# Performance work log

Measured on AMD Instinct MI355X. Metric: run time of the kernel, lower is better.

The kernel has to match this reference:

```python
import jax, jax.numpy as jnp
import numpy as np

B, T, D = 4, 2048, 1024
H = 16
HD = D // H  # 64


def setup_inputs() -> dict:
    key = jax.random.key(0)
    ks = jax.random.split(key, 6)
    s = 0.02
    x = jax.random.normal(ks[0], (B, T, D), dtype=jnp.float32)
    # per-head projection weights, stored stacked: [H, HD, D] (torch Linear weight layout)
    Wq = jax.random.normal(ks[1], (H, HD, D), dtype=jnp.float32) * s
    Wk = jax.random.normal(ks[2], (H, HD, D), dtype=jnp.float32) * s
    Wv = jax.random.normal(ks[3], (H, HD, D), dtype=jnp.float32) * s
    Wo = jax.random.normal(ks[4], (D, D), dtype=jnp.float32) * s  # proj weight [out, in]
    bo = jax.random.normal(ks[5], (D,), dtype=jnp.float32) * s
    return {"x": x, "Wq": Wq, "Wk": Wk, "Wv": Wv, "Wo": Wo, "bo": bo}


def reference(x, Wq, Wk, Wv, Wo, bo):
    Bx, Tx, _ = x.shape
    # project: [B,T,D] x [H,HD,D] -> [B,H,T,HD]
    q = jnp.einsum('btd,hed->bhte', x, Wq)
    k = jnp.einsum('btd,hed->bhte', x, Wk)
    v = jnp.einsum('btd,hed->bhte', x, Wv)
    scale = 1.0 / jnp.sqrt(jnp.array(q.shape[-1], dtype=x.dtype))
    scores = jnp.einsum('bhte,bhse->bhts', q, k) * scale  # [B,H,T,T]
    causal = jnp.tril(jnp.ones((Tx, Tx), dtype=bool))
    scores = jnp.where(causal, scores, jnp.array(-jnp.inf, dtype=scores.dtype))
    weights = jax.nn.softmax(scores, axis=-1)
    out = jnp.einsum('bhts,bhse->bhte', weights, v)  # [B,H,T,HD]
    # concat heads (head h occupies contiguous slice, matching torch.cat order)
    out = out.transpose(0, 2, 1, 3).reshape(Bx, Tx, -1)  # [B,T,D]
    out = out @ Wo.T + bo
    return out
```

## Files before the change

### kernel.cpp

```cpp
#include <hip/hip_runtime.h>
#include <cstdint>
#include <cstddef>

typedef unsigned short u16;
typedef float  f32x4  __attribute__((ext_vector_type(4)));
typedef __bf16 bf16x8 __attribute__((ext_vector_type(8)));
typedef unsigned short us8 __attribute__((ext_vector_type(8)));
typedef unsigned short us4 __attribute__((ext_vector_type(4)));
typedef float  f32x4v __attribute__((ext_vector_type(4)));
typedef unsigned int u32x2 __attribute__((ext_vector_type(2)));

#define AS1 __attribute__((address_space(1)))
#define AS3 __attribute__((address_space(3)))

__device__ __forceinline__ u16 f2b(float f) {
  unsigned u = __float_as_uint(f);
  u += 0x7FFFu + ((u >> 16) & 1u);
  return (u16)(u >> 16);
}

__device__ __forceinline__ unsigned pkbf(float a, float b) {
  unsigned ua = __float_as_uint(a) + 0x8000u;
  unsigned ub = __float_as_uint(b) + 0x8000u;
  return __builtin_amdgcn_perm(ub, ua, 0x07060302u);
}

__device__ __forceinline__ unsigned cvtpk(float a, float b) {
  unsigned short lo = __builtin_bit_cast(unsigned short, (__bf16)a);
  unsigned short hi = __builtin_bit_cast(unsigned short, (__bf16)b);
  return (unsigned)lo | ((unsigned)hi << 16);
}

__device__ __forceinline__ bf16x8 ldfrag(const u16* p) {
  us8 v = *(const us8*)p;
  return __builtin_bit_cast(bf16x8, v);
}

__device__ __forceinline__ f32x4 mfma16(bf16x8 a, bf16x8 b, f32x4 c) {
  return __builtin_amdgcn_mfma_f32_16x16x32_bf16(a, b, c, 0, 0, 0);
}

__device__ __forceinline__ void gl_lds16(const u16* g, AS3 u16* l) {
  __builtin_amdgcn_global_load_lds((AS1 void*)g, (AS3 void*)l, 16, 0, 0);
}


__global__ __launch_bounds__(256) void cvt_all(
    const float* __restrict__ x,
    const float* __restrict__ Wq, const float* __restrict__ Wk,
    const float* __restrict__ Wv, const float* __restrict__ Wo,
    u16* __restrict__ xb, u16* __restrict__ Wqkv, u16* __restrict__ Wob) {
  for (int blk = blockIdx.x; blk < 12288; blk += 3072) {
    const float* s;
    u16* d;
    int i;
    if (blk < 8192)       { s = x;  d = xb;             i = blk * 256 + threadIdx.x; }
    else if (blk < 9216)  { s = Wq; d = Wqkv;           i = (blk - 8192) * 256 + threadIdx.x; }
    else if (blk < 10240) { s = Wk; d = Wqkv + 1048576; i = (blk - 9216) * 256 + threadIdx.x; }
    else if (blk < 11264) { s = Wv; d = Wqkv + 2097152; i = (blk - 10240) * 256 + threadIdx.x; }
    else                  { s = Wo; d = Wob;            i = (blk - 11264) * 256 + threadIdx.x; }
    f32x4v f = ((const f32x4v*)s)[i];
    us4 o = { f2b(f[0]), f2b(f[1]), f2b(f[2]), f2b(f[3]) };
    ((us4*)d)[i] = o;
  }
}

__global__ __launch_bounds__(256) void gemm_qkv(
    const u16* __restrict__ A, const u16* __restrict__ W,
    u16* __restrict__ Qb, u16* __restrict__ Kb, u16* __restrict__ Vt) {
  __shared__ u16 lA[128 * 64];
  __shared__ u16 lB[128 * 64];
  const int tid = threadIdx.x;
  const int lane = tid & 63, wave = tid >> 6;
  const int quad = lane >> 4, l16 = lane & 15;
  const int wr = wave >> 1, wc = wave & 1;

  const int p = blockIdx.x;
  const int l = (p & 7) * 64 + (p >> 3);
  const int by = l >> 3;
  const int bx0 = l & 7;
  const int m0 = by * 128;

  AS3 u16* lA3 = (AS3 u16*)lA;
  AS3 u16* lB3 = (AS3 u16*)lB;
  const int g3 = (((lane & 7) ^ (lane >> 3)) * 8);
  const int srow = lane >> 3;
  const int pA = ((quad) ^ (l16 & 7)) * 8;
  const int pB = ((4 + quad) ^ (l16 & 7)) * 8;

  const u16* gA = A + (size_t)(m0 + wave * 8 + srow) * 1024 + g3;

#pragma unroll 1
  for (int sec = 0; sec < 3; sec++) {
    const int n0 = (bx0 + sec * 8) * 128;
    const u16* gB = W + (size_t)(n0 + wave * 8 + srow) * 1024 + g3;
    f32x4 acc[4][4] = {};

    for (int k0 = 0; k0 < 1024; k0 += 64) {
      __syncthreads();
#pragma unroll
      for (int i = 0; i < 4; i++) {
        gl_lds16(gA + (size_t)i * 32768 + k0, lA3 + (i * 4 + wave) * 512);
        gl_lds16(gB + (size_t)i * 32768 + k0, lB3 + (i * 4 + wave) * 512);
      }
      __syncthreads();
#pragma unroll
      for (int kk = 0; kk < 2; kk++) {
        const int pk = kk ? pB : pA;
        bf16x8 aF[4], bF[4];
#pragma unroll
        for (int mt = 0; mt < 4; mt++)
          aF[mt] = ldfrag(&lA[(wr * 64 + mt * 16 + l16) * 64 + pk]);
#pragma unroll
        for (int nt = 0; nt < 4; nt++)
          bF[nt] = ldfrag(&lB[(wc * 64 + nt * 16 + l16) * 64 + pk]);
        if (sec != 2) {
#pragma unroll
          for (int mt = 0; mt < 4; mt++)
#pragma unroll
            for (int nt = 0; nt < 4; nt++)
              acc[mt][nt] = mfma16(bF[nt], aF[mt], acc[mt][nt]);
        } else {
#pragma unroll
          for (int mt = 0; mt < 4; mt++)
#pragma unroll
            for (int nt = 0; nt < 4; nt++)
              acc[mt][nt] = mfma16(aF[mt], bF[nt], acc[mt][nt]);
        }
      }
    }

    if (sec != 2) {
      const float qsc = (sec == 0) ? 0.180336880111120426f : 1.0f;
      u16* __restrict__ D = (sec == 0) ? Qb : Kb;
      const int hb = ((n0 & 1023) >> 6) + wc;
#pragma unroll
      for (int mt = 0; mt < 4; mt++) {
        int t = m0 + wr * 64 + mt * 16 + l16;
        int b = t >> 11, tt = t & 2047;
        size_t rowb = (((size_t)b * 16 + hb) * 2048 + tt) * 64;
#pragma unroll
        for (int nt = 0; nt < 4; nt++) {
          int e = nt * 16 + quad * 4;
          u32x2 pk = { pkbf(acc[mt][nt][0] * qsc, acc[mt][nt][1] * qsc),
                       pkbf(acc[mt][nt][2] * qsc, acc[mt][nt][3] * qsc) };
          *(u32x2*)&D[rowb + e] = pk;
        }
      }
    } else {
#pragma unroll
      for (int mt = 0; mt < 4; mt++) {
        int t = m0 + wr * 64 + mt * 16 + quad * 4;
        int b = t >> 11, tt = t & 2047;
#pragma unroll
        for (int nt = 0; nt < 4; nt++) {
          int ns = (n0 & 1023) + wc * 64 + nt * 16 + l16;
          int h = ns >> 6, e = ns & 63;
          size_t addr = (((size_t)b * 16 + h) * 64 + e) * 2048 + tt;
          u32x2 pk = { pkbf(acc[mt][nt][0], acc[mt][nt][1]),
                       pkbf(acc[mt][nt][2], acc[mt][nt][3]) };
          *(u32x2*)&Vt[addr] = pk;
        }
      }
    }
  }
}

__global__ __launch_bounds__(512, 4) void attn(
    const u16* __restrict__ Q, const u16* __restrict__ K,
    const u16* __restrict__ Vt, u16* __restrict__ O) {
  __shared__ u16 lK[128 * 64];
  __shared__ u16 lV[64 * 128];
  __shared__ u16 lP[8 * 16 * 40];
  const int tid = threadIdx.x;
  const int lane = tid & 63, wave = tid >> 6;
  const int quad = lane >> 4, l16 = lane & 15;
  const int bh = blockIdx.x;
  const int pidx = blockIdx.y;
  const size_t base = (size_t)bh * (2048 * 64);
  u16* lPw = lP + wave * 640;
  const int b = bh >> 4, h = bh & 15;
  AS3 u16* lK3 = (AS3 u16*)lK;
  AS3 u16* lV3 = (AS3 u16*)lV;

  const int g3 = ((lane & 7) ^ (lane >> 3)) * 8;
  const u16* gK = K + base + (size_t)(wave * 16 + (lane >> 3)) * 64 + g3;
  const int er = lane >> 4, p16 = lane & 15;
  const int e0 = wave * 8 + er, e1 = wave * 8 + 4 + er;
  const u16* gV0 = Vt + base + (size_t)e0 * 2048 + ((p16 ^ (e0 & 7)) * 8);
  const u16* gV1 = Vt + base + (size_t)e1 * 2048 + ((p16 ^ (e1 & 7)) * 8);

  const int e7 = l16 & 7;
  const int pq0 = (quad ^ e7) * 8;
  const int pq1 = ((4 + quad) ^ e7) * 8;

  us8 ones_u = { 0x3F80, 0x3F80, 0x3F80, 0x3F80, 0x3F80, 0x3F80, 0x3F80, 0x3F80 };
  const bf16x8 onesA = __builtin_bit_cast(bf16x8, ones_u);

  for (int half = 0; half < 2; half++) {
    const int qb = half ? pidx : (15 - pidx);
    const int t0 = qb << 7;
    const int tq = t0 + wave * 16 + l16;
    const bf16x8 qF0 = ldfrag(Q + base + (size_t)tq * 64 + quad * 8);
    const bf16x8 qF1 = ldfrag(Q + base + (size_t)tq * 64 + 32 + quad * 8);
    float l_i = 0.f;
    f32x4 o[4] = {};

    for (int j = 0; j <= qb; j++) {
      const int s0 = j << 7;
      __syncthreads();
      gl_lds16(gK + (size_t)s0 * 64,       lK3 + wave * 1024);
      gl_lds16(gK + (size_t)s0 * 64 + 512, lK3 + wave * 1024 + 512);
      gl_lds16(gV0 + s0, lV3 + wave * 1024);
      gl_lds16(gV1 + s0, lV3 + wave * 1024 + 512);
      __syncthreads();

      f32x4 S[8];
      __builtin_amdgcn_s_setprio(1);
#pragma unroll
      for (int nt = 0; nt < 8; nt++) {
        int sr = nt * 16 + l16;
        f32x4 a = {};
        a = mfma16(ldfrag(&lK[sr * 64 + pq0]), qF0, a);
        a = mfma16(ldfrag(&lK[sr * 64 + pq1]), qF1, a);
        S[nt] = a;
      }
      __builtin_amdgcn_s_setprio(0);

      if (j == qb) {
#pragma unroll
        for (int nt = 0; nt < 8; nt++)
#pragma unroll
          for (int r = 0; r < 4; r++) {
            int s = s0 + nt * 16 + quad * 4 + r;
            if (s > tq) S[nt][r] = -INFINITY;
          }
      }

#pragma unroll
      for (int nt = 0; nt < 8; nt++)
#pragma unroll
        for (int r = 0; r < 4; r++)
          S[nt][r] = __builtin_amdgcn_exp2f(S[nt][r]);

      f32x4 ol = {};
#pragma unroll
      for (int c = 0; c < 4; c++) {
        u32x2 d0 = { cvtpk(S[2*c][0],   S[2*c][1]),   cvtpk(S[2*c][2],   S[2*c][3]) };
        u32x2 d1 = { cvtpk(S[2*c+1][0], S[2*c+1][1]), cvtpk(S[2*c+1][2], S[2*c+1][3]) };
        *(u32x2*)&lPw[l16 * 40 + quad * 4]      = d0;
        *(u32x2*)&lPw[l16 * 40 + 16 + quad * 4] = d1;
        __asm__ volatile("s_waitcnt lgkmcnt(0)" ::: "memory");
        bf16x8 bP = ldfrag(&lPw[l16 * 40 + quad * 8]);
        __builtin_amdgcn_s_setprio(1);
#pragma unroll
        for (int ot = 0; ot < 4; ot++) {
          int pos = ((c * 4 + quad) ^ e7) * 8;
          o[ot] = mfma16(ldfrag(&lV[(ot * 16 + l16) * 128 + pos]), bP, o[ot]);
        }
        ol = mfma16(onesA, bP, ol);
        __builtin_amdgcn_s_setprio(0);
      }
      l_i += ol[0];
    }

    const float inv = 1.f / l_i;
#pragma unroll
    for (int ot = 0; ot < 4; ot++) {
      u32x2 pk = { cvtpk(o[ot][0] * inv, o[ot][1] * inv),
                   cvtpk(o[ot][2] * inv, o[ot][3] * inv) };
      *(u32x2*)&O[((size_t)b * 2048 + tq) * 1024 + h * 64 + ot * 16 + quad * 4] = pk;
    }
  }
}

__global__ __launch_bounds__(256) void gemm_out(
    const u16* __restrict__ A, const u16* __restrict__ W,
    const float* __restrict__ bias, float* __restrict__ out) {
  __shared__ u16 lA[128 * 64];
  __shared__ u16 lB[128 * 64];
  const int tid = threadIdx.x;
  const int lane = tid & 63, wave = tid >> 6;
  const int quad = lane >> 4, l16 = lane & 15;
  const int wr = wave >> 1, wc = wave & 1;
  const int m0 = blockIdx.y * 128;
  const int n0 = blockIdx.x * 128;
  AS3 u16* lA3 = (AS3 u16*)lA;
  AS3 u16* lB3 = (AS3 u16*)lB;
  f32x4 acc[4][4] = {};
  const int g3 = (((lane & 7) ^ (lane >> 3)) * 8);
  const int srow = lane >> 3;
  const int pA = ((quad) ^ (l16 & 7)) * 8;
  const int pB = ((4 + quad) ^ (l16 & 7)) * 8;
  const u16* gA = A + (size_t)(m0 + wave * 8 + srow) * 1024 + g3;
  const u16* gB = W + (size_t)(n0 + wave * 8 + srow) * 1024 + g3;

  for (int k0 = 0; k0 < 1024; k0 += 64) {
    __syncthreads();
#pragma unroll
    for (int i = 0; i < 4; i++) {
      gl_lds16(gA + (size_t)i * 32768 + k0, lA3 + (i * 4 + wave) * 512);
      gl_lds16(gB + (size_t)i * 32768 + k0, lB3 + (i * 4 + wave) * 512);
    }
    __syncthreads();
#pragma unroll
    for (int kk = 0; kk < 2; kk++) {
      const int pk = kk ? pB : pA;
      bf16x8 aF[4], bF[4];
#pragma unroll
      for (int mt = 0; mt < 4; mt++)
        aF[mt] = ldfrag(&lA[(wr * 64 + mt * 16 + l16) * 64 + pk]);
#pragma unroll
      for (int nt = 0; nt < 4; nt++)
        bF[nt] = ldfrag(&lB[(wc * 64 + nt * 16 + l16) * 64 + pk]);
#pragma unroll
      for (int mt = 0; mt < 4; mt++)
#pragma unroll
        for (int nt = 0; nt < 4; nt++)
          acc[mt][nt] = mfma16(aF[mt], bF[nt], acc[mt][nt]);
    }
  }

#pragma unroll
  for (int mt = 0; mt < 4; mt++) {
#pragma unroll
    for (int nt = 0; nt < 4; nt++) {
#pragma unroll
      for (int r = 0; r < 4; r++) {
        int m = m0 + wr * 64 + mt * 16 + quad * 4 + r;
        int n = n0 + wc * 64 + nt * 16 + l16;
        out[(size_t)m * 1024 + n] = acc[mt][nt][r] + bias[n];
      }
    }
  }
}

extern "C" void kernel_launch(void* const* d_in, const int* in_sizes, int n_in,
                              void* d_out, int out_size, void* d_ws, size_t ws_size,
                              hipStream_t stream) {
  const float* x  = (const float*)d_in[0];
  const float* Wq = (const float*)d_in[1];
  const float* Wk = (const float*)d_in[2];
  const float* Wv = (const float*)d_in[3];
  const float* Wo = (const float*)d_in[4];
  const float* bo = (const float*)d_in[5];
  float* out = (float*)d_out;

  u16* ws   = (u16*)d_ws;
  u16* xb   = ws;
  u16* Wqkv = ws + 8388608;
  u16* Wob  = ws + 11534336;
  u16* Qb   = ws + 12582912;
  u16* Ao   = xb;
  u16* Kb   = (u16*)d_out;
  u16* Vt   = Kb + 8388608;

  cvt_all<<<3072, 256, 0, stream>>>(x, Wq, Wk, Wv, Wo, xb, Wqkv, Wob);
  gemm_qkv<<<512, 256, 0, stream>>>(xb, Wqkv, Qb, Kb, Vt);
  attn<<<dim3(64, 8), 512, 0, stream>>>(Qb, Kb, Vt, Ao);
  gemm_out<<<dim3(8, 64), 256, 0, stream>>>(Ao, Wob, bo, out);
}
```

Measured before the change: 236.4 us.

## Double-buffer LDS in QKV and output GEMMs to overlap loads with MFMA

Both projection GEMMs now use two LDS buffers: the global-to-LDS load for the next K-tile is issued before computing on the current one, with one vmcnt wait and barrier per step instead of two syncthreads. The QKV GEMM flattens its three sections and sixteen K-steps into a single 48-step pipelined loop, so loads also run ahead across the section epilogue boundaries. This is meant to hide global load latency behind MFMA work. In exchange LDS per block doubles to 64KB, which may lower occupancy, and the waits rely on hand-placed sched barriers.

```diff
diff --git a/kernel.cpp b/kernel.cpp
--- a/kernel.cpp
+++ b/kernel.cpp
@@ -43,6 +43,9 @@
 __device__ __forceinline__ void gl_lds16(const u16* g, AS3 u16* l) {
   __builtin_amdgcn_global_load_lds((AS1 void*)g, (AS3 void*)l, 16, 0, 0);
 }
+
+#define SBAR0() __builtin_amdgcn_sched_barrier(0)
+#define WVM0()  do { __asm__ volatile("s_waitcnt vmcnt(0)" ::: "memory"); SBAR0(); } while (0)
 
 
 __global__ __launch_bounds__(256) void cvt_all(
@@ -68,8 +71,8 @@
 __global__ __launch_bounds__(256) void gemm_qkv(
     const u16* __restrict__ A, const u16* __restrict__ W,
     u16* __restrict__ Qb, u16* __restrict__ Kb, u16* __restrict__ Vt) {
-  __shared__ u16 lA[128 * 64];
-  __shared__ u16 lB[128 * 64];
+  __shared__ u16 lA[2 * 128 * 64];
+  __shared__ u16 lB[2 * 128 * 64];
   const int tid = threadIdx.x;
   const int lane = tid & 63, wave = tid >> 6;
   const int quad = lane >> 4, l16 = lane & 15;
@@ -89,81 +92,105 @@
   const int pB = ((4 + quad) ^ (l16 & 7)) * 8;
 
   const u16* gA = A + (size_t)(m0 + wave * 8 + srow) * 1024 + g3;
+  const u16* gW = W + (size_t)(wave * 8 + srow) * 1024 + g3;
+
+#define STAGE_T(T) do {                                                     \
+    int sec_ = (T) >> 4;                                                    \
+    int k0_ = ((T) & 15) * 64;                                              \
+    int bo_ = ((T) & 1) * 8192;                                             \
+    const u16* gBp_ = gW + (size_t)((bx0 + sec_ * 8) * 128) * 1024 + k0_;   \
+    const u16* gAp_ = gA + k0_;                                             \
+    _Pragma("unroll") for (int i_ = 0; i_ < 4; i_++) {                      \
+      gl_lds16(gAp_ + (size_t)i_ * 32768, lA3 + bo_ + (i_ * 4 + wave) * 512); \
+      gl_lds16(gBp_ + (size_t)i_ * 32768, lB3 + bo_ + (i_ * 4 + wave) * 512); \
+    }                                                                       \
+    SBAR0();                                                                \
+  } while (0)
+
+  f32x4 acc[4][4] = {};
+
+  STAGE_T(0);
+  WVM0();
+  __builtin_amdgcn_s_barrier();
+  SBAR0();
 
 #pragma unroll 1
-  for (int sec = 0; sec < 3; sec++) {
-    const int n0 = (bx0 + sec * 8) * 128;
-    const u16* gB = W + (size_t)(n0 + wave * 8 + srow) * 1024 + g3;
-    f32x4 acc[4][4] = {};
-
-    for (int k0 = 0; k0 < 1024; k0 += 64) {
-      __syncthreads();
-#pragma unroll
-      for (int i = 0; i < 4; i++) {
-        gl_lds16(gA + (size_t)i * 32768 + k0, lA3 + (i * 4 + wave) * 512);
-        gl_lds16(gB + (size_t)i * 32768 + k0, lB3 + (i * 4 + wave) * 512);
-      }
-      __syncthreads();
-#pragma unroll
-      for (int kk = 0; kk < 2; kk++) {
-        const int pk = kk ? pB : pA;
-        bf16x8 aF[4], bF[4];
+  for (int T = 0; T < 48; T++) {
+    if (T < 47) STAGE_T(T + 1);
+    const int sec = T >> 4;
+    const u16* bA = lA + (T & 1) * 8192;
+    const u16* bB = lB + (T & 1) * 8192;
+#pragma unroll
+    for (int kk = 0; kk < 2; kk++) {
+      const int pk = kk ? pB : pA;
+      bf16x8 aF[4], bF[4];
+#pragma unroll
+      for (int mt = 0; mt < 4; mt++)
+        aF[mt] = ldfrag(&bA[(wr * 64 + mt * 16 + l16) * 64 + pk]);
+#pragma unroll
+      for (int nt = 0; nt < 4; nt++)
+        bF[nt] = ldfrag(&bB[(wc * 64 + nt * 16 + l16) * 64 + pk]);
+      if (sec != 2) {
 #pragma unroll
         for (int mt = 0; mt < 4; mt++)
-          aF[mt] = ldfrag(&lA[(wr * 64 + mt * 16 + l16) * 64 + pk]);
+#pragma unroll
+          for (int nt = 0; nt < 4; nt++)
+            acc[mt][nt] = mfma16(bF[nt], aF[mt], acc[mt][nt]);
+      } else {
+#pragma unroll
+        for (int mt = 0; mt < 4; mt++)
+#pragma unroll
+          for (int nt = 0; nt < 4; nt++)
+            acc[mt][nt] = mfma16(aF[mt], bF[nt], acc[mt][nt]);
+      }
+    }
+    WVM0();
+    __builtin_amdgcn_s_barrier();
+    SBAR0();
+
+    if ((T & 15) == 15) {
+      const int n0 = (bx0 + sec * 8) * 128;
+      if (sec != 2) {
+        const float qsc = (sec == 0) ? 0.180336880111120426f : 1.0f;
+        u16* __restrict__ D = (sec == 0) ? Qb : Kb;
+        const int hb = ((n0 & 1023) >> 6) + wc;
+#pragma unroll
+        for (int mt = 0; mt < 4; mt++) {
+          int t = m0 + wr * 64 + mt * 16 + l16;
+          int b = t >> 11, tt = t & 2047;
+          size_t rowb = (((size_t)b * 16 + hb) * 2048 + tt) * 64;
+#pragma unroll
+          for (int nt = 0; nt < 4; nt++) {
+            int e = nt * 16 + quad * 4;
+            u32x2 pk = { pkbf(acc[mt][nt][0] * qsc, acc[mt][nt][1] * qsc),
+                         pkbf(acc[mt][nt][2] * qsc, acc[mt][nt][3] * qsc) };
+            *(u32x2*)&D[rowb + e] = pk;
+          }
+        }
+      } else {
+#pragma unroll
+        for (int mt = 0; mt < 4; mt++) {
+          int t = m0 + wr * 64 + mt * 16 + quad * 4;
+          int b = t >> 11, tt = t & 2047;
+#pragma unroll
+          for (int nt = 0; nt < 4; nt++) {
+            int ns = (n0 & 1023) + wc * 64 + nt * 16 + l16;
+            int h = ns >> 6, e = ns & 63;
+            size_t addr = (((size_t)b * 16 + h) * 64 + e) * 2048 + tt;
+            u32x2 pk = { pkbf(acc[mt][nt][0], acc[mt][nt][1]),
+                         pkbf(acc[mt][nt][2], acc[mt][nt][3]) };
+            *(u32x2*)&Vt[addr] = pk;
+          }
+        }
+      }
+#pragma unroll
+      for (int mt = 0; mt < 4; mt++)
 #pragma unroll
         for (int nt = 0; nt < 4; nt++)
-          bF[nt] = ldfrag(&lB[(wc * 64 + nt * 16 + l16) * 64 + pk]);
-        if (sec != 2) {
-#pragma unroll
-          for (int mt = 0; mt < 4; mt++)
-#pragma unroll
-            for (int nt = 0; nt < 4; nt++)
-              acc[mt][nt] = mfma16(bF[nt], aF[mt], acc[mt][nt]);
-        } else {
-#pragma unroll
-          for (int mt = 0; mt < 4; mt++)
-#pragma unroll
-            for (int nt = 0; nt < 4; nt++)
-              acc[mt][nt] = mfma16(aF[mt], bF[nt], acc[mt][nt]);
-        }
-      }
-    }
-
-    if (sec != 2) {
-      const float qsc = (sec == 0) ? 0.180336880111120426f : 1.0f;
-      u16* __restrict__ D = (sec == 0) ? Qb : Kb;
-      const int hb = ((n0 & 1023) >> 6) + wc;
-#pragma unroll
-      for (int mt = 0; mt < 4; mt++) {
-        int t = m0 + wr * 64 + mt * 16 + l16;
-        int b = t >> 11, tt = t & 2047;
-        size_t rowb = (((size_t)b * 16 + hb) * 2048 + tt) * 64;
-#pragma unroll
-        for (int nt = 0; nt < 4; nt++) {
-          int e = nt * 16 + quad * 4;
-          u32x2 pk = { pkbf(acc[mt][nt][0] * qsc, acc[mt][nt][1] * qsc),
-                       pkbf(acc[mt][nt][2] * qsc, acc[mt][nt][3] * qsc) };
-          *(u32x2*)&D[rowb + e] = pk;
-        }
-      }
-    } else {
-#pragma unroll
-      for (int mt = 0; mt < 4; mt++) {
-        int t = m0 + wr * 64 + mt * 16 + quad * 4;
-        int b = t >> 11, tt = t & 2047;
-#pragma unroll
-        for (int nt = 0; nt < 4; nt++) {
-          int ns = (n0 & 1023) + wc * 64 + nt * 16 + l16;
-          int h = ns >> 6, e = ns & 63;
-          size_t addr = (((size_t)b * 16 + h) * 64 + e) * 2048 + tt;
-          u32x2 pk = { pkbf(acc[mt][nt][0], acc[mt][nt][1]),
-                       pkbf(acc[mt][nt][2], acc[mt][nt][3]) };
-          *(u32x2*)&Vt[addr] = pk;
-        }
-      }
+          acc[mt][nt] = (f32x4){0.f, 0.f, 0.f, 0.f};
     }
   }
+#undef STAGE_T
 }
 
 __global__ __launch_bounds__(512, 4) void attn(
@@ -277,8 +304,8 @@
 __global__ __launch_bounds__(256) void gemm_out(
     const u16* __restrict__ A, const u16* __restrict__ W,
     const float* __restrict__ bias, float* __restrict__ out) {
-  __shared__ u16 lA[128 * 64];
-  __shared__ u16 lB[128 * 64];
+  __shared__ u16 lA[2 * 128 * 64];
+  __shared__ u16 lB[2 * 128 * 64];
   const int tid = threadIdx.x;
   const int lane = tid & 63, wave = tid >> 6;
   const int quad = lane >> 4, l16 = lane & 15;
@@ -295,31 +322,47 @@
   const u16* gA = A + (size_t)(m0 + wave * 8 + srow) * 1024 + g3;
   const u16* gB = W + (size_t)(n0 + wave * 8 + srow) * 1024 + g3;
 
-  for (int k0 = 0; k0 < 1024; k0 += 64) {
-    __syncthreads();
-#pragma unroll
-    for (int i = 0; i < 4; i++) {
-      gl_lds16(gA + (size_t)i * 32768 + k0, lA3 + (i * 4 + wave) * 512);
-      gl_lds16(gB + (size_t)i * 32768 + k0, lB3 + (i * 4 + wave) * 512);
-    }
-    __syncthreads();
+#define STAGE_O(T) do {                                                     \
+    int k0_ = (T) * 64;                                                     \
+    int bo_ = ((T) & 1) * 8192;                                             \
+    _Pragma("unroll") for (int i_ = 0; i_ < 4; i_++) {                      \
+      gl_lds16(gA + (size_t)i_ * 32768 + k0_, lA3 + bo_ + (i_ * 4 + wave) * 512); \
+      gl_lds16(gB + (size_t)i_ * 32768 + k0_, lB3 + bo_ + (i_ * 4 + wave) * 512); \
+    }                                                                       \
+    SBAR0();                                                                \
+  } while (0)
+
+  STAGE_O(0);
+  WVM0();
+  __builtin_amdgcn_s_barrier();
+  SBAR0();
+
+#pragma unroll 1
+  for (int T = 0; T < 16; T++) {
+    if (T < 15) STAGE_O(T + 1);
+    const u16* bA = lA + (T & 1) * 8192;
+    const u16* bB = lB + (T & 1) * 8192;
 #pragma unroll
     for (int kk = 0; kk < 2; kk++) {
       const int pk = kk ? pB : pA;
       bf16x8 aF[4], bF[4];
 #pragma unroll
       for (int mt = 0; mt < 4; mt++)
-        aF[mt] = ldfrag(&lA[(wr * 64 + mt * 16 + l16) * 64 + pk]);
+        aF[mt] = ldfrag(&bA[(wr * 64 + mt * 16 + l16) * 64 + pk]);
 #pragma unroll
       for (int nt = 0; nt < 4; nt++)
-        bF[nt] = ldfrag(&lB[(wc * 64 + nt * 16 + l16) * 64 + pk]);
+        bF[nt] = ldfrag(&bB[(wc * 64 + nt * 16 + l16) * 64 + pk]);
 #pragma unroll
       for (int mt = 0; mt < 4; mt++)
 #pragma unroll
         for (int nt = 0; nt < 4; nt++)
           acc[mt][nt] = mfma16(aF[mt], bF[nt], acc[mt][nt]);
     }
+    WVM0();
+    __builtin_amdgcn_s_barrier();
+    SBAR0();
   }
+#undef STAGE_O
 
 #pragma unroll
   for (int mt = 0; mt < 4; mt++) {
```

New measurement: 254.2 us. 1.08x slower.
